# Kernel optimization log

Hardware: AMD Instinct MI355X
Metric: run time of the kernel (lower is better)

The kernel has to match this reference:

```python
import jax, jax.numpy as jnp
import numpy as np

L, H, P = 8192, 1024, 512
DT_MIN, DT_MAX = 1e-3, 1e-1
CONJ_SYM = True


def setup_inputs() -> dict:
    key = jax.random.key(0)
    ks = jax.random.split(key, 6)
    input_sequence = jax.random.normal(ks[0], (L, H), jnp.float32)
    # HiPPO-DPLR-like eigenvalues: negative real part, linearly spaced imag part
    Lambda_re = -0.5 * jnp.ones((P,), jnp.float32)
    Lambda_im = jnp.pi * jnp.arange(P, dtype=jnp.float32)
    # B param stacks real/imag in last dim: (P, H, 2); C: (H, P, 2)
    B = jax.random.normal(ks[1], (P, H, 2), jnp.float32) / np.float32(np.sqrt(2 * H))
    C = jax.random.normal(ks[2], (H, P, 2), jnp.float32) / np.float32(np.sqrt(2 * P))
    D = jax.random.normal(ks[3], (H,), jnp.float32)
    log_step = jax.random.uniform(ks[4], (P,), jnp.float32,
                                  minval=np.float32(np.log(DT_MIN)),
                                  maxval=np.float32(np.log(DT_MAX)))
    return dict(input_sequence=input_sequence, Lambda_re=Lambda_re,
                Lambda_im=Lambda_im, B=B, C=C, D=D, log_step=log_step)


def _binop(e_i, e_j):
    # diagonal LTI composition: (A, b) o (A', b') = (A'A, A'b + b')
    A_i, b_i = e_i
    A_j, b_j = e_j
    return A_j * A_i, A_j * b_i + b_j


def _forward(input_sequence, Lambda_re, Lambda_im, B, C, D, log_step):
    Lambda = Lambda_re + 1j * Lambda_im                  # (P,) complex
    B_tilde = B[..., 0] + 1j * B[..., 1]                 # (P, H)
    C_tilde = C[..., 0] + 1j * C[..., 1]                 # (H, P)
    step = jnp.exp(log_step)                             # (P,)  step_rescale = 1.0
    # ZOH discretization
    Lambda_bar = jnp.exp(Lambda * step)                  # (P,)
    B_bar = ((1.0 / Lambda) * (Lambda_bar - 1.0))[:, None] * B_tilde  # (P, H)
    # input projection, vectorized over L: Bu[l] = B_bar @ u[l]
    Bu = input_sequence.astype(B_bar.dtype) @ B_bar.T    # (L, P) complex
    Lambda_elems = jnp.broadcast_to(Lambda_bar, Bu.shape)  # (L, P)
    _, xs = jax.lax.associative_scan(_binop, (Lambda_elems, Bu))  # states (L, P)
    mult = 2.0 if CONJ_SYM else 1.0
    ys = mult * jnp.einsum('lp,hp->lh', xs, C_tilde).real  # (L, H)
    out = ys + D * input_sequence                          # D-skip
    return out, xs[-1]


def reference(input_sequence, Lambda_re, Lambda_im, B, C, D, log_step):
    return _forward(input_sequence, Lambda_re, Lambda_im, B, C, D, log_step)
```

## Files before the change

kernel.cpp:

```cpp
#include <hip/hip_runtime.h>
#include <hip/hip_bf16.h>
#include <hip/hip_fp16.h>
#include <stdint.h>

typedef _Float16 f16;
typedef __attribute__((ext_vector_type(8))) _Float16 half8;
typedef __attribute__((ext_vector_type(4))) _Float16 half4;
typedef __attribute__((ext_vector_type(4))) float f32x4;

#define L_SEQ 8192
#define H_DIM 1024
#define P_DIM 512
#define NB 256
#define TT 32

#define GL16(gp, lp)                                                        \
  __builtin_amdgcn_global_load_lds(                                          \
      (const __attribute__((address_space(1))) void*)(gp),                   \
      (__attribute__((address_space(3))) void*)(lp), 16, 0, 0)

__global__ void k_consts(const float* __restrict__ lre, const float* __restrict__ lim,
                         const float* __restrict__ lstep, float* __restrict__ cst) {
  int p = threadIdx.x;
  double step = exp((double)lstep[p]);
  double ar = (double)lre[p] * step, ai = (double)lim[p] * step;
  double er = exp(ar);
  double lbr = er * cos(ai), lbi = er * sin(ai);
  double nr = lbr - 1.0, ni = lbi;
  double d = (double)lre[p] * (double)lre[p] + (double)lim[p] * (double)lim[p];
  double gr = (nr * (double)lre[p] + ni * (double)lim[p]) / d;
  double gi = (ni * (double)lre[p] - nr * (double)lim[p]) / d;
  cst[p] = (float)lbr; cst[512 + p] = (float)lbi;
  cst[1024 + p] = (float)gr; cst[1536 + p] = (float)gi;
  double aT = ai * (double)TT;
  double eT = exp(ar * (double)TT);
  cst[2048 + p] = (float)(eT * cos(aT));
  cst[2560 + p] = (float)(eT * sin(aT));
  double gm = fmax(fabs(gr), fabs(gi));
  int e = ilogb(gm) + 1;
  float sc = ldexpf(1.0f, e);
  cst[3072 + p] = sc;
  cst[3072 + 512 + p] = sc;
  cst[4096 + p] = ldexpf(1.0f, -e);
}

__global__ void k_w1(const float* __restrict__ B, const float* __restrict__ cst,
                     f16* __restrict__ W1) {
  int idx = blockIdx.x * 256 + threadIdx.x;
  int n = idx >> 10, k = idx & 1023;
  int p = n & 511;
  float b0 = B[(size_t)(p * 1024 + k) * 2];
  float b1 = B[(size_t)(p * 1024 + k) * 2 + 1];
  float gr = cst[1024 + p], gi = cst[1536 + p];
  float inv = cst[4096 + p];
  float re = (gr * b0 - gi * b1) * inv;
  float im = (gr * b1 + gi * b0) * inv;
  W1[idx] = (f16)((n < 512) ? re : im);
}

__global__ void k_w2(const float* __restrict__ C, f16* __restrict__ W2) {
  int idx = blockIdx.x * 256 + threadIdx.x;
  int h = idx >> 10, k = idx & 1023;
  float v = (k < 512) ? 2.0f * C[(size_t)(h * 512 + k) * 2]
                      : -2.0f * C[(size_t)(h * 512 + (k - 512)) * 2 + 1];
  W2[idx] = (f16)v;
}

__global__ void k_cvt(const float* __restrict__ u, f16* __restrict__ uh) {
  int i = blockIdx.x * 256 + threadIdx.x;
  float4 v = reinterpret_cast<const float4*>(u)[i];
  half4 h;
  h.x = (f16)v.x; h.y = (f16)v.y; h.z = (f16)v.z; h.w = (f16)v.w;
  reinterpret_cast<half4*>(uh)[i] = h;
}

template <int EPI>
__global__ __launch_bounds__(256) void k_gemm(const f16* __restrict__ A,
                                              const f16* __restrict__ Bm,
                                              float* __restrict__ Cm,
                                              const float* __restrict__ D,
                                              const float* __restrict__ U,
                                              const float* __restrict__ S) {
  __shared__ f16 As[128 * 32];
  __shared__ f16 Bs[128 * 32];
  const int tid = threadIdx.x;
  const int wave = tid >> 6, lane = tid & 63;
  const int bm = blockIdx.x >> 3, bn = blockIdx.x & 7;
  const int m0 = bm * 128, n0 = bn * 128;
  const int wr = (wave >> 1) * 64, wc = (wave & 1) * 64;
  const int lr = lane & 15, lg = lane >> 4;
  f32x4 acc[4][4] = {};

  const int c0 = wave * 64 + lane;
  const int c1 = c0 + 256;
  const int ar0 = c0 >> 2, ak0 = (c0 & 3) * 8;
  const int ar1 = c1 >> 2, ak1 = (c1 & 3) * 8;
  char* lA0 = (char*)As + wave * 1024;
  char* lA1 = (char*)As + 4096 + wave * 1024;
  char* lB0 = (char*)Bs + wave * 1024;
  char* lB1 = (char*)Bs + 4096 + wave * 1024;

  for (int kt = 0; kt < 32; ++kt) {
    const int k0 = kt * 32;
    GL16(A + (size_t)(m0 + ar0) * 1024 + k0 + ak0, lA0);
    GL16(A + (size_t)(m0 + ar1) * 1024 + k0 + ak1, lA1);
    GL16(Bm + (size_t)(n0 + ar0) * 1024 + k0 + ak0, lB0);
    GL16(Bm + (size_t)(n0 + ar1) * 1024 + k0 + ak1, lB1);
    __syncthreads();
    half8 af[4], bf[4];
#pragma unroll
    for (int m = 0; m < 4; ++m)
      af[m] = *(const half8*)&As[(wr + m * 16 + lr) * 32 + lg * 8];
#pragma unroll
    for (int n = 0; n < 4; ++n)
      bf[n] = *(const half8*)&Bs[(wc + n * 16 + lr) * 32 + lg * 8];
#pragma unroll
    for (int m = 0; m < 4; ++m)
#pragma unroll
      for (int n = 0; n < 4; ++n)
        acc[m][n] = __builtin_amdgcn_mfma_f32_16x16x32_f16(af[m], bf[n], acc[m][n], 0, 0, 0);
    __syncthreads();
  }

#pragma unroll
  for (int m = 0; m < 4; ++m)
#pragma unroll
    for (int n = 0; n < 4; ++n) {
      int row = m0 + wr + m * 16 + lg * 4;
      int col = n0 + wc + n * 16 + lr;
      float* cp = Cm + (size_t)row * 1024 + col;
      float scale = (EPI == 0) ? S[col] : 0.0f;
#pragma unroll
      for (int j = 0; j < 4; ++j) {
        float v = acc[m][n][j];
        if (EPI) v += D[col] * U[(size_t)(row + j) * 1024 + col];
        else v *= scale;
        cp[(size_t)j * 1024] = v;
      }
    }
}

__global__ void k_scanA(const float* __restrict__ Bu, const float* __restrict__ cst,
                        float* __restrict__ carry) {
  int p = threadIdx.x;
  int b = blockIdx.x;
  float lbr = cst[p], lbi = cst[512 + p];
  float xr = 0.f, xi = 0.f;
  const float* row = Bu + (size_t)b * TT * 1024;
  for (int t = 0; t < TT; ++t) {
    float br = row[t * 1024 + p], bi = row[t * 1024 + 512 + p];
    float nxr = lbr * xr - lbi * xi + br;
    float nxi = lbr * xi + lbi * xr + bi;
    xr = nxr; xi = nxi;
  }
  carry[b * 1024 + p] = xr;
  carry[b * 1024 + 512 + p] = xi;
}

__global__ void k_scanB(const float* __restrict__ carry, const float* __restrict__ cst,
                        float* __restrict__ prefix) {
  int p = threadIdx.x;
  float lTr = cst[2048 + p], lTi = cst[2560 + p];
  float xr = 0.f, xi = 0.f;
  for (int b = 0; b < NB; ++b) {
    prefix[b * 1024 + p] = xr;
    prefix[b * 1024 + 512 + p] = xi;
    float cr = carry[b * 1024 + p], ci = carry[b * 1024 + 512 + p];
    float nr = lTr * xr - lTi * xi + cr;
    float ni = lTr * xi + lTi * xr + ci;
    xr = nr; xi = ni;
  }
}

__global__ void k_scanC(const float* __restrict__ Bu, const float* __restrict__ cst,
                        const float* __restrict__ prefix, f16* __restrict__ X,
                        float* __restrict__ fin, int tail) {
  int p = threadIdx.x;
  int b = blockIdx.x;
  float lbr = cst[p], lbi = cst[512 + p];
  float xr = prefix[b * 1024 + p], xi = prefix[b * 1024 + 512 + p];
  const float* row = Bu + (size_t)b * TT * 1024;
  f16* xrow = X + (size_t)b * TT * 1024;
  for (int t = 0; t < TT; ++t) {
    float br = row[t * 1024 + p], bi = row[t * 1024 + 512 + p];
    float nxr = lbr * xr - lbi * xi + br;
    float nxi = lbr * xi + lbi * xr + bi;
    xr = nxr; xi = nxi;
    xrow[t * 1024 + p] = (f16)xr;
    xrow[t * 1024 + 512 + p] = (f16)xi;
  }
  if (b == NB - 1) {
    if (tail >= 1024) {
      fin[2 * p] = xr;
      fin[2 * p + 1] = xi;
    } else if (tail >= 512) {
      fin[p] = xr;
    }
  }
}

extern "C" void kernel_launch(void* const* d_in, const int* in_sizes, int n_in,
                              void* d_out, int out_size, void* d_ws, size_t ws_size,
                              hipStream_t stream) {
  const float* u    = (const float*)d_in[0];
  const float* lre  = (const float*)d_in[1];
  const float* lim  = (const float*)d_in[2];
  const float* B    = (const float*)d_in[3];
  const float* C    = (const float*)d_in[4];
  const float* D    = (const float*)d_in[5];
  const float* lstp = (const float*)d_in[6];
  float* out = (float*)d_out;
  int tail = out_size - L_SEQ * H_DIM;

  char* ws = (char*)d_ws;
  float* cst   = (float*)(ws + 0);
  f16* uh      = (f16*)(ws + 32768);
  f16* W1      = (f16*)(ws + 16809984);
  f16* W2      = (f16*)(ws + 18907136);
  float* Bu    = (float*)(ws + 21004288);
  f16* Xc      = (f16*)(ws + 54558720);
  float* carry = (float*)(ws + 71335936);
  float* prefix= (float*)(ws + 72384512);

  k_consts<<<1, 512, 0, stream>>>(lre, lim, lstp, cst);
  k_w1<<<4096, 256, 0, stream>>>(B, cst, W1);
  k_w2<<<4096, 256, 0, stream>>>(C, W2);
  k_cvt<<<8192, 256, 0, stream>>>(u, uh);
  k_gemm<0><<<512, 256, 0, stream>>>(uh, W1, Bu, nullptr, nullptr, cst + 3072);
  k_scanA<<<NB, 512, 0, stream>>>(Bu, cst, carry);
  k_scanB<<<1, 512, 0, stream>>>(carry, cst, prefix);
  k_scanC<<<NB, 512, 0, stream>>>(Bu, cst, prefix, Xc, out + (size_t)L_SEQ * H_DIM, tail);
  k_gemm<1><<<512, 256, 0, stream>>>(Xc, W2, out, D, u, nullptr);
}
```

Baseline: 208.0 us.

## Store Bu in f16, parallelize carry scan, merge prep kernels

Fuses the weight-preparation and input-conversion kernels into one launch, stores the intermediate Bu projection in f16 instead of f32, and replaces the single-block serial carry scan with a per-channel Hillis-Steele scan using precomputed powers of Lambda_bar. The D-skip epilogue now reads the f16 copy of the input. This cuts memory traffic, launch count, and a serial bottleneck, at the cost of reduced precision in Bu and the skip term.

```diff
diff --git a/kernel.cpp b/kernel.cpp
--- a/kernel.cpp
+++ b/kernel.cpp
@@ -32,54 +32,59 @@
   double gi = (ni * (double)lre[p] - nr * (double)lim[p]) / d;
   cst[p] = (float)lbr; cst[512 + p] = (float)lbi;
   cst[1024 + p] = (float)gr; cst[1536 + p] = (float)gi;
-  double aT = ai * (double)TT;
-  double eT = exp(ar * (double)TT);
-  cst[2048 + p] = (float)(eT * cos(aT));
-  cst[2560 + p] = (float)(eT * sin(aT));
+#pragma unroll
+  for (int s = 0; s < 8; ++s) {
+    double n = 32.0 * (double)(1 << s);
+    double eT = exp(ar * n);
+    cst[3072 + s * 1024 + p]       = (float)(eT * cos(ai * n));
+    cst[3072 + s * 1024 + 512 + p] = (float)(eT * sin(ai * n));
+  }
   double gm = fmax(fabs(gr), fabs(gi));
   int e = ilogb(gm) + 1;
   float sc = ldexpf(1.0f, e);
-  cst[3072 + p] = sc;
-  cst[3072 + 512 + p] = sc;
-  cst[4096 + p] = ldexpf(1.0f, -e);
-}
-
-__global__ void k_w1(const float* __restrict__ B, const float* __restrict__ cst,
-                     f16* __restrict__ W1) {
-  int idx = blockIdx.x * 256 + threadIdx.x;
-  int n = idx >> 10, k = idx & 1023;
-  int p = n & 511;
-  float b0 = B[(size_t)(p * 1024 + k) * 2];
-  float b1 = B[(size_t)(p * 1024 + k) * 2 + 1];
-  float gr = cst[1024 + p], gi = cst[1536 + p];
-  float inv = cst[4096 + p];
-  float re = (gr * b0 - gi * b1) * inv;
-  float im = (gr * b1 + gi * b0) * inv;
-  W1[idx] = (f16)((n < 512) ? re : im);
-}
-
-__global__ void k_w2(const float* __restrict__ C, f16* __restrict__ W2) {
-  int idx = blockIdx.x * 256 + threadIdx.x;
-  int h = idx >> 10, k = idx & 1023;
-  float v = (k < 512) ? 2.0f * C[(size_t)(h * 512 + k) * 2]
-                      : -2.0f * C[(size_t)(h * 512 + (k - 512)) * 2 + 1];
-  W2[idx] = (f16)v;
-}
-
-__global__ void k_cvt(const float* __restrict__ u, f16* __restrict__ uh) {
-  int i = blockIdx.x * 256 + threadIdx.x;
-  float4 v = reinterpret_cast<const float4*>(u)[i];
-  half4 h;
-  h.x = (f16)v.x; h.y = (f16)v.y; h.z = (f16)v.z; h.w = (f16)v.w;
-  reinterpret_cast<half4*>(uh)[i] = h;
+  cst[11264 + p] = sc;
+  cst[11264 + 512 + p] = sc;
+  cst[12288 + p] = ldexpf(1.0f, -e);
+}
+
+__global__ void k_prep(const float* __restrict__ B, const float* __restrict__ C,
+                       const float* __restrict__ u, const float* __restrict__ cst,
+                       f16* __restrict__ W1, f16* __restrict__ W2,
+                       f16* __restrict__ uh) {
+  int blk = blockIdx.x;
+  if (blk < 4096) {
+    int idx = blk * 256 + threadIdx.x;
+    int n = idx >> 10, k = idx & 1023;
+    int p = n & 511;
+    float b0 = B[(size_t)(p * 1024 + k) * 2];
+    float b1 = B[(size_t)(p * 1024 + k) * 2 + 1];
+    float gr = cst[1024 + p], gi = cst[1536 + p];
+    float inv = cst[12288 + p];
+    float re = (gr * b0 - gi * b1) * inv;
+    float im = (gr * b1 + gi * b0) * inv;
+    W1[idx] = (f16)((n < 512) ? re : im);
+  } else if (blk < 8192) {
+    int idx = (blk - 4096) * 256 + threadIdx.x;
+    int h = idx >> 10, k = idx & 1023;
+    float v = (k < 512) ? 2.0f * C[(size_t)(h * 512 + k) * 2]
+                        : -2.0f * C[(size_t)(h * 512 + (k - 512)) * 2 + 1];
+    W2[idx] = (f16)v;
+  } else {
+    int i = (blk - 8192) * 256 + threadIdx.x;
+    float4 v = reinterpret_cast<const float4*>(u)[i];
+    half4 h;
+    h.x = (f16)v.x; h.y = (f16)v.y; h.z = (f16)v.z; h.w = (f16)v.w;
+    reinterpret_cast<half4*>(uh)[i] = h;
+  }
 }
 
 template <int EPI>
 __global__ __launch_bounds__(256) void k_gemm(const f16* __restrict__ A,
                                               const f16* __restrict__ Bm,
-                                              float* __restrict__ Cm,
+                                              float* __restrict__ CmF,
+                                              f16* __restrict__ CmH,
                                               const float* __restrict__ D,
-                                              const float* __restrict__ U,
+                                              const f16* __restrict__ Uh,
                                               const float* __restrict__ S) {
   __shared__ f16 As[128 * 32];
   __shared__ f16 Bs[128 * 32];
@@ -128,27 +133,29 @@
     for (int n = 0; n < 4; ++n) {
       int row = m0 + wr + m * 16 + lg * 4;
       int col = n0 + wc + n * 16 + lr;
-      float* cp = Cm + (size_t)row * 1024 + col;
       float scale = (EPI == 0) ? S[col] : 0.0f;
 #pragma unroll
       for (int j = 0; j < 4; ++j) {
         float v = acc[m][n][j];
-        if (EPI) v += D[col] * U[(size_t)(row + j) * 1024 + col];
-        else v *= scale;
-        cp[(size_t)j * 1024] = v;
+        if (EPI) {
+          v += D[col] * (float)Uh[(size_t)(row + j) * 1024 + col];
+          CmF[(size_t)(row + j) * 1024 + col] = v;
+        } else {
+          CmH[(size_t)(row + j) * 1024 + col] = (f16)(v * scale);
+        }
       }
     }
 }
 
-__global__ void k_scanA(const float* __restrict__ Bu, const float* __restrict__ cst,
+__global__ void k_scanA(const f16* __restrict__ Bu, const float* __restrict__ cst,
                         float* __restrict__ carry) {
   int p = threadIdx.x;
   int b = blockIdx.x;
   float lbr = cst[p], lbi = cst[512 + p];
   float xr = 0.f, xi = 0.f;
-  const float* row = Bu + (size_t)b * TT * 1024;
+  const f16* row = Bu + (size_t)b * TT * 1024;
   for (int t = 0; t < TT; ++t) {
-    float br = row[t * 1024 + p], bi = row[t * 1024 + 512 + p];
+    float br = (float)row[t * 1024 + p], bi = (float)row[t * 1024 + 512 + p];
     float nxr = lbr * xr - lbi * xi + br;
     float nxi = lbr * xi + lbi * xr + bi;
     xr = nxr; xi = nxi;
@@ -159,30 +166,42 @@
 
 __global__ void k_scanB(const float* __restrict__ carry, const float* __restrict__ cst,
                         float* __restrict__ prefix) {
-  int p = threadIdx.x;
-  float lTr = cst[2048 + p], lTi = cst[2560 + p];
-  float xr = 0.f, xi = 0.f;
-  for (int b = 0; b < NB; ++b) {
-    prefix[b * 1024 + p] = xr;
-    prefix[b * 1024 + 512 + p] = xi;
-    float cr = carry[b * 1024 + p], ci = carry[b * 1024 + 512 + p];
-    float nr = lTr * xr - lTi * xi + cr;
-    float ni = lTr * xi + lTi * xr + ci;
-    xr = nr; xi = ni;
-  }
-}
-
-__global__ void k_scanC(const float* __restrict__ Bu, const float* __restrict__ cst,
+  __shared__ float sre[256], sim[256];
+  int p = blockIdx.x;
+  int b = threadIdx.x;
+  float xr = carry[b * 1024 + p], xi = carry[b * 1024 + 512 + p];
+  sre[b] = xr; sim[b] = xi;
+  __syncthreads();
+#pragma unroll
+  for (int s = 0; s < 8; ++s) {
+    float pr = cst[3072 + s * 1024 + p];
+    float pi = cst[3072 + s * 1024 + 512 + p];
+    int off = 1 << s;
+    float ar = 0.f, ai = 0.f;
+    if (b >= off) { ar = sre[b - off]; ai = sim[b - off]; }
+    __syncthreads();
+    xr += pr * ar - pi * ai;
+    xi += pr * ai + pi * ar;
+    sre[b] = xr; sim[b] = xi;
+    __syncthreads();
+  }
+  float er = 0.f, ei = 0.f;
+  if (b > 0) { er = sre[b - 1]; ei = sim[b - 1]; }
+  prefix[b * 1024 + p] = er;
+  prefix[b * 1024 + 512 + p] = ei;
+}
+
+__global__ void k_scanC(const f16* __restrict__ Bu, const float* __restrict__ cst,
                         const float* __restrict__ prefix, f16* __restrict__ X,
                         float* __restrict__ fin, int tail) {
   int p = threadIdx.x;
   int b = blockIdx.x;
   float lbr = cst[p], lbi = cst[512 + p];
   float xr = prefix[b * 1024 + p], xi = prefix[b * 1024 + 512 + p];
-  const float* row = Bu + (size_t)b * TT * 1024;
+  const f16* row = Bu + (size_t)b * TT * 1024;
   f16* xrow = X + (size_t)b * TT * 1024;
   for (int t = 0; t < TT; ++t) {
-    float br = row[t * 1024 + p], bi = row[t * 1024 + 512 + p];
+    float br = (float)row[t * 1024 + p], bi = (float)row[t * 1024 + 512 + p];
     float nxr = lbr * xr - lbi * xi + br;
     float nxi = lbr * xi + lbi * xr + bi;
     xr = nxr; xi = nxi;
@@ -214,21 +233,19 @@
 
   char* ws = (char*)d_ws;
   float* cst   = (float*)(ws + 0);
-  f16* uh      = (f16*)(ws + 32768);
-  f16* W1      = (f16*)(ws + 16809984);
-  f16* W2      = (f16*)(ws + 18907136);
-  float* Bu    = (float*)(ws + 21004288);
-  f16* Xc      = (f16*)(ws + 54558720);
-  float* carry = (float*)(ws + 71335936);
-  float* prefix= (float*)(ws + 72384512);
+  f16* uh      = (f16*)(ws + 65536);
+  f16* W1      = (f16*)(ws + 16842752);
+  f16* W2      = (f16*)(ws + 18939904);
+  f16* Bu      = (f16*)(ws + 21037056);
+  f16* Xc      = (f16*)(ws + 37814272);
+  float* carry = (float*)(ws + 54591488);
+  float* prefix= (float*)(ws + 55639040);
 
   k_consts<<<1, 512, 0, stream>>>(lre, lim, lstp, cst);
-  k_w1<<<4096, 256, 0, stream>>>(B, cst, W1);
-  k_w2<<<4096, 256, 0, stream>>>(C, W2);
-  k_cvt<<<8192, 256, 0, stream>>>(u, uh);
-  k_gemm<0><<<512, 256, 0, stream>>>(uh, W1, Bu, nullptr, nullptr, cst + 3072);
+  k_prep<<<16384, 256, 0, stream>>>(B, C, u, cst, W1, W2, uh);
+  k_gemm<0><<<512, 256, 0, stream>>>(uh, W1, nullptr, Bu, nullptr, nullptr, cst + 11264);
   k_scanA<<<NB, 512, 0, stream>>>(Bu, cst, carry);
-  k_scanB<<<1, 512, 0, stream>>>(carry, cst, prefix);
+  k_scanB<<<512, 256, 0, stream>>>(carry, cst, prefix);
   k_scanC<<<NB, 512, 0, stream>>>(Bu, cst, prefix, Xc, out + (size_t)L_SEQ * H_DIM, tail);
-  k_gemm<1><<<512, 256, 0, stream>>>(Xc, W2, out, D, u, nullptr);
-}
+  k_gemm<1><<<512, 256, 0, stream>>>(Xc, W2, out, nullptr, D, uh, nullptr);
+}
```

Result: faster. 184.1 us (-11.5%).
